# Optimization experiments

Measured on AMD Instinct MI355X. Metric: run time of the kernel, lower is better.

The kernel has to match this reference:

```python
import jax, jax.numpy as jnp
import numpy as np
from itertools import product

DIM = 384
HEADS = 8
DIM_HEAD = 64
INNER = HEADS * DIM_HEAD  # 512
KS = 3                    # kernel_size (attention window)
PAD = KS // 2
W_WIN = KS * KS           # 9
SCALE = DIM_HEAD ** -0.5


def setup_inputs() -> dict:
    key = jax.random.key(0)
    k1, k2, k3, k4, k5 = jax.random.split(key, 5)
    B, H, W = 4, 56, 56
    x = jax.random.normal(k1, (B, DIM, H, W), dtype=jnp.float32)
    # 1x1 conv weights stored as (out_ch, in_ch)
    Wq = jax.random.normal(k2, (INNER, DIM), dtype=jnp.float32) * (DIM ** -0.5)
    Wkv = jax.random.normal(k3, (2 * INNER, DIM), dtype=jnp.float32) * (DIM ** -0.5)
    Wo = jax.random.normal(k4, (DIM, INNER), dtype=jnp.float32) * (INNER ** -0.5)
    bo = jax.random.normal(k5, (DIM,), dtype=jnp.float32) * 0.01
    return {"x": x, "Wq": Wq, "Wkv": Wkv, "Wo": Wo, "bo": bo}


def _conv1x1(x, w):
    # x: (B,Cin,H,W), w: (Cout,Cin) -> (B,Cout,H,W)
    return jnp.einsum('bchw,oc->bohw', x, w)


def reference(x, Wq, Wkv, Wo, bo):
    B, C, H, W = x.shape
    q = _conv1x1(x, Wq)                       # (B, INNER, H, W)
    kv = _conv1x1(x, Wkv)                     # (B, 2*INNER, H, W)
    k, v = jnp.split(kv, 2, axis=1)
    # split channels heads-major, matching torch reshape (B, heads, dh, H, W)
    q = q.reshape(B, HEADS, DIM_HEAD, H, W)
    k = k.reshape(B, HEADS, DIM_HEAD, H, W)
    v = v.reshape(B, HEADS, DIM_HEAD, H, W)
    # zero-pad spatial dims (matches F.unfold zero padding: padded taps get logit 0)
    k_pad = jnp.pad(k, ((0, 0), (0, 0), (0, 0), (PAD, PAD), (PAD, PAD)))
    v_pad = jnp.pad(v, ((0, 0), (0, 0), (0, 0), (PAD, PAD), (PAD, PAD)))
    offsets = list(product(range(KS), range(KS)))  # row-major = unfold order
    # dots: (B, heads, H, W, w)
    dots = jnp.stack([
        jnp.einsum('bhdxy,bhdxy->bhxy', q, k_pad[:, :, :, i:i + H, j:j + W])
        for (i, j) in offsets
    ], axis=-1) * SCALE
    attn = jax.nn.softmax(dots, axis=-1)      # softmax over the 9-tap window
    # weighted sum of shifted v: (B, heads, dh, H, W)
    out = sum(
        attn[:, :, None, :, :, w_idx] * v_pad[:, :, :, i:i + H, j:j + W]
        for w_idx, (i, j) in enumerate(offsets)
    )
    out = out.reshape(B, INNER, H, W)
    return _conv1x1(out, Wo) + bo[None, :, None, None]
```

## Files before the change

### kernel.cpp

```cpp
#include <hip/hip_runtime.h>


#define HW 3136
#define WIMG 56
#define QKV_CH 1536
#define SCALE 0.125f
#define SLEN 200

typedef __bf16 bf16x8_t __attribute__((ext_vector_type(8)));
typedef float f32x4_t __attribute__((ext_vector_type(4)));

__device__ __forceinline__ float bf2f(unsigned short u) {
    return __uint_as_float(((unsigned int)u) << 16);
}
__device__ __forceinline__ unsigned short f2bf(float f) {
    unsigned int u = __float_as_uint(f);
    u += 0x7FFFu + ((u >> 16) & 1u);
    return (unsigned short)(u >> 16);
}

__global__ __launch_bounds__(256) void cvt_w(
    const float* __restrict__ Wq, const float* __restrict__ Wkv,
    const float* __restrict__ Wo,
    unsigned short* __restrict__ wT, unsigned short* __restrict__ wT3)
{
    const int i = blockIdx.x * 256 + threadIdx.x;
    if (i < 73728) {
        const int g = i & 3;
        const int idx3 = i >> 2;
        const int o128 = idx3 & 127;
        const int rest = idx3 >> 7;
        const int kb = rest % 12, oblk = rest / 12;
        const int o = oblk * 128 + o128;
        const int k0 = kb * 32 + g * 8;
        const float* src = (o < 512) ? (Wq + (size_t)o * 384 + k0)
                                     : (Wkv + (size_t)(o - 512) * 384 + k0);
        const float4 v0 = *reinterpret_cast<const float4*>(src);
        const float4 v1 = *reinterpret_cast<const float4*>(src + 4);
        uint4 u;
        u.x = (unsigned int)f2bf(v0.x) | ((unsigned int)f2bf(v0.y) << 16);
        u.y = (unsigned int)f2bf(v0.z) | ((unsigned int)f2bf(v0.w) << 16);
        u.z = (unsigned int)f2bf(v1.x) | ((unsigned int)f2bf(v1.y) << 16);
        u.w = (unsigned int)f2bf(v1.z) | ((unsigned int)f2bf(v1.w) << 16);
        reinterpret_cast<uint4*>(wT)[i] = u;
    } else {
        const int j = i - 73728;
        const int g = j & 3;
        const int idx3 = j >> 2;
        const int o128 = idx3 & 127;
        const int rest = idx3 >> 7;
        const int kb = rest % 16, oblk = rest / 16;
        const int o = oblk * 128 + o128;
        const float* src = Wo + (size_t)o * 512 + kb * 32 + g * 8;
        const float4 v0 = *reinterpret_cast<const float4*>(src);
        const float4 v1 = *reinterpret_cast<const float4*>(src + 4);
        uint4 u;
        u.x = (unsigned int)f2bf(v0.x) | ((unsigned int)f2bf(v0.y) << 16);
        u.y = (unsigned int)f2bf(v0.z) | ((unsigned int)f2bf(v0.w) << 16);
        u.z = (unsigned int)f2bf(v1.x) | ((unsigned int)f2bf(v1.y) << 16);
        u.w = (unsigned int)f2bf(v1.z) | ((unsigned int)f2bf(v1.w) << 16);
        reinterpret_cast<uint4*>(wT3)[j] = u;
    }
}

__global__ __launch_bounds__(256) void cvtT_x(
    const float* __restrict__ x, unsigned short* __restrict__ xT)
{
    __shared__ unsigned short Tl[64 * 36];
    const int sblk = blockIdx.x, kblk = blockIdx.y, b = blockIdx.z;
    const int t = threadIdx.x;

    if (sblk == 49) {
        unsigned short* dst = xT + (((size_t)b * 25 + 24) * 12 + kblk) * 4096 + 2048;
        *reinterpret_cast<uint4*>(dst + t * 8) = (uint4){0, 0, 0, 0};
        return;
    }

    const float* xp = x + ((size_t)b * 384 + (size_t)kblk * 32) * HW + sblk * 64;
    const int c = t >> 3;
#pragma unroll
    for (int i = 0; i < 2; i++) {
        const int sc = (t & 7) + 8 * i;
        const float4 v = *reinterpret_cast<const float4*>(xp + (size_t)c * HW + sc * 4);
        const int s4 = sc * 4;
        Tl[(s4 + 0) * 36 + c] = f2bf(v.x);
        Tl[(s4 + 1) * 36 + c] = f2bf(v.y);
        Tl[(s4 + 2) * 36 + c] = f2bf(v.z);
        Tl[(s4 + 3) * 36 + c] = f2bf(v.w);
    }
    __syncthreads();

    const int row = t >> 2, gran = t & 3;
    const uint2 lo = *reinterpret_cast<const uint2*>(&Tl[row * 36 + gran * 8]);
    const uint2 hi = *reinterpret_cast<const uint2*>(&Tl[row * 36 + gran * 8 + 4]);
    uint4 o; o.x = lo.x; o.y = lo.y; o.z = hi.x; o.w = hi.y;
    unsigned short* dst = xT + (((size_t)b * 25 + (sblk >> 1)) * 12 + kblk) * 4096
                        + (sblk & 1) * 2048;
    *reinterpret_cast<uint4*>(dst + t * 8) = o;
}

__global__ __launch_bounds__(256) void gemm1(
    const unsigned short* __restrict__ xT,
    const unsigned short* __restrict__ wT,
    unsigned short* __restrict__ qkv)
{
    __shared__ __align__(16) unsigned short A_lds[128 * 32];
    __shared__ __align__(16) unsigned short B_lds[128 * 32];

    const int sblk = blockIdx.x;
    const int oblk = blockIdx.y;
    const int b  = blockIdx.z;
    const int t  = threadIdx.x;
    const int lane = t & 63, w = t >> 6;
    const int quad = lane >> 4, mrow = lane & 15;
    const int wm = w >> 1, wn = w & 1;

    const unsigned short* wsrc = wT + ((size_t)oblk * 12) * 4096;
    const unsigned short* xsrc = xT + (((size_t)b * 25 + sblk) * 12) * 4096;

    f32x4_t acc[4][4];
#pragma unroll
    for (int m = 0; m < 4; m++)
#pragma unroll
        for (int n = 0; n < 4; n++) acc[m][n] = (f32x4_t){0.f, 0.f, 0.f, 0.f};

    for (int kb = 0; kb < 12; kb++) {
        const uint4 a0 = *reinterpret_cast<const uint4*>(wsrc + (size_t)kb * 4096 + t * 8);
        const uint4 a1 = *reinterpret_cast<const uint4*>(wsrc + (size_t)kb * 4096 + 2048 + t * 8);
        const uint4 b0 = *reinterpret_cast<const uint4*>(xsrc + (size_t)kb * 4096 + t * 8);
        const uint4 b1 = *reinterpret_cast<const uint4*>(xsrc + (size_t)kb * 4096 + 2048 + t * 8);

        __syncthreads();
        *reinterpret_cast<uint4*>(A_lds + t * 8) = a0;
        *reinterpret_cast<uint4*>(A_lds + 2048 + t * 8) = a1;
        *reinterpret_cast<uint4*>(B_lds + t * 8) = b0;
        *reinterpret_cast<uint4*>(B_lds + 2048 + t * 8) = b1;
        __syncthreads();

        bf16x8_t af[4], bf[4];
#pragma unroll
        for (int m = 0; m < 4; m++)
            af[m] = *reinterpret_cast<const bf16x8_t*>(&A_lds[(wm * 64 + m * 16 + mrow) * 32 + quad * 8]);
#pragma unroll
        for (int n = 0; n < 4; n++)
            bf[n] = *reinterpret_cast<const bf16x8_t*>(&B_lds[(wn * 64 + n * 16 + mrow) * 32 + quad * 8]);
#pragma unroll
        for (int m = 0; m < 4; m++)
#pragma unroll
            for (int n = 0; n < 4; n++)
                acc[m][n] = __builtin_amdgcn_mfma_f32_16x16x32_bf16(af[m], bf[n], acc[m][n], 0, 0, 0);
    }

    const int o0 = oblk * 128 + wm * 64;
    const int s0 = sblk * 128 + wn * 64;
    unsigned short* outb = qkv + (size_t)b * QKV_CH * HW;
#pragma unroll
    for (int m = 0; m < 4; m++)
#pragma unroll
        for (int n = 0; n < 4; n++) {
            const int ss = s0 + n * 16 + mrow;
            if (ss < HW) {
#pragma unroll
                for (int r = 0; r < 4; r++) {
                    const int oo = o0 + m * 16 + quad * 4 + r;
                    outb[(size_t)oo * HW + ss] = f2bf(acc[m][n][r]);
                }
            }
        }
}

__global__ __launch_bounds__(256) void natt2(
    const unsigned short* __restrict__ qkv,
    unsigned short* __restrict__ aoT)
{
    __shared__ __align__(16) unsigned short smem[2 * 64 * SLEN];
    unsigned short* Kl = smem;
    unsigned short* Vl = smem + 64 * SLEN;
    float* dred = reinterpret_cast<float*>(smem);

    const int t = threadIdx.x, lane = t & 63, w = t >> 6;
    const int sblk = blockIdx.x;
    const int s0 = sblk * 64;
    const int s  = s0 + lane;
    const int h  = blockIdx.y, b = blockIdx.z;
    const int y  = s / WIMG, xx = s % WIMG;

    const size_t hbase = (size_t)b * QKV_CH * HW + (size_t)(h * 64) * HW;
    const unsigned short* kg = qkv + hbase + (size_t)512 * HW;
    const unsigned short* vg = qkv + hbase + (size_t)1024 * HW;

#pragma unroll
    for (int i = 0; i < 6; i++) {
        const int f = i * 256 + t;
        const int d = f / 24, j = f % 24;
        int g = s0 - 64 + j * 8;
        g = min(max(g, 0), HW - 8);
        const uint4 k4 = *reinterpret_cast<const uint4*>(kg + (size_t)d * HW + g);
        const uint4 v4 = *reinterpret_cast<const uint4*>(vg + (size_t)d * HW + g);
        *reinterpret_cast<uint4*>(&Kl[d * SLEN + j * 8]) = k4;
        *reinterpret_cast<uint4*>(&Vl[d * SLEN + j * 8]) = v4;
    }

    int   off9[9];
    float msk[9];
#pragma unroll
    for (int ty = 0; ty < 3; ty++)
#pragma unroll
        for (int tx = 0; tx < 3; tx++) {
            const int tap = ty * 3 + tx;
            const int ny = y + ty - 1, nx = xx + tx - 1;
            const bool v = (ny >= 0) && (ny < WIMG) && (nx >= 0) && (nx < WIMG);
            off9[tap] = v ? ((ty - 1) * WIMG + (tx - 1)) : 0;
            msk[tap]  = v ? 1.f : 0.f;
        }

    __syncthreads();

    const unsigned short* qp = qkv + hbase + s;
    float dots[9];
#pragma unroll
    for (int tp = 0; tp < 9; tp++) dots[tp] = 0.f;
#pragma unroll 4
    for (int dd = 0; dd < 16; dd++) {
        const int d = w * 16 + dd;
        const float qv = bf2f(qp[(size_t)d * HW]);
        const int bi = d * SLEN + lane + 64;
#pragma unroll
        for (int tp = 0; tp < 9; tp++)
            dots[tp] += qv * bf2f(Kl[bi + off9[tp]]);
    }

    __syncthreads();
#pragma unroll
    for (int tp = 0; tp < 9; tp++) dred[(tp * 4 + w) * 64 + lane] = dots[tp];
    __syncthreads();

    float mx = -1e30f, dt[9];
#pragma unroll
    for (int tp = 0; tp < 9; tp++) {
        const float sum = dred[(tp * 4 + 0) * 64 + lane] + dred[(tp * 4 + 1) * 64 + lane] +
                          dred[(tp * 4 + 2) * 64 + lane] + dred[(tp * 4 + 3) * 64 + lane];
        dt[tp] = msk[tp] * (sum * SCALE);
        mx = fmaxf(mx, dt[tp]);
    }
    float se = 0.f, w9[9];
#pragma unroll
    for (int tp = 0; tp < 9; tp++) { w9[tp] = __expf(dt[tp] - mx); se += w9[tp]; }
    const float inv = 1.f / se;
#pragma unroll
    for (int tp = 0; tp < 9; tp++) w9[tp] *= inv * msk[tp];

    __align__(16) unsigned short ov[16];
#pragma unroll 4
    for (int dd = 0; dd < 16; dd++) {
        const int d = w * 16 + dd;
        const int bi = d * SLEN + lane + 64;
        float o = 0.f;
#pragma unroll
        for (int tp = 0; tp < 9; tp++)
            o += w9[tp] * bf2f(Vl[bi + off9[tp]]);
        ov[dd] = f2bf(o);
    }
    unsigned short* dst = aoT + (((size_t)(b * 49 + sblk)) * 16 + (h * 2 + (w >> 1))) * 2048
                        + lane * 32 + (w & 1) * 16;
    *reinterpret_cast<uint4*>(dst)     = *reinterpret_cast<const uint4*>(ov);
    *reinterpret_cast<uint4*>(dst + 8) = *reinterpret_cast<const uint4*>(ov + 8);
}

__global__ __launch_bounds__(256) void gemm3(
    const unsigned short* __restrict__ aoT,
    const unsigned short* __restrict__ wT3,
    const float* __restrict__ bias,
    float* __restrict__ out)
{
    __shared__ __align__(16) unsigned short A_lds[128 * 32];
    __shared__ __align__(16) unsigned short B_lds[64 * 32];

    const int sblk = blockIdx.x;
    const int oblk = blockIdx.y;
    const int b  = blockIdx.z;
    const int t  = threadIdx.x;
    const int lane = t & 63, w = t >> 6;
    const int quad = lane >> 4, mrow = lane & 15;
    const int wm = w >> 1, wn = w & 1;

    const unsigned short* asrc = wT3 + (size_t)oblk * 16 * 4096;
    const unsigned short* bsrc = aoT + ((size_t)(b * 49 + sblk)) * 16 * 2048;

    f32x4_t acc[4][2];
#pragma unroll
    for (int m = 0; m < 4; m++)
#pragma unroll
        for (int n = 0; n < 2; n++) acc[m][n] = (f32x4_t){0.f, 0.f, 0.f, 0.f};

    for (int kb = 0; kb < 16; kb++) {
        const uint4 a0 = *reinterpret_cast<const uint4*>(asrc + (size_t)kb * 4096 + t * 8);
        const uint4 a1 = *reinterpret_cast<const uint4*>(asrc + (size_t)kb * 4096 + 2048 + t * 8);
        const uint4 b0 = *reinterpret_cast<const uint4*>(bsrc + (size_t)kb * 2048 + t * 8);

        __syncthreads();
        *reinterpret_cast<uint4*>(A_lds + t * 8) = a0;
        *reinterpret_cast<uint4*>(A_lds + 2048 + t * 8) = a1;
        *reinterpret_cast<uint4*>(B_lds + t * 8) = b0;
        __syncthreads();

        bf16x8_t af[4], bf[2];
#pragma unroll
        for (int m = 0; m < 4; m++)
            af[m] = *reinterpret_cast<const bf16x8_t*>(&A_lds[(wm * 64 + m * 16 + mrow) * 32 + quad * 8]);
#pragma unroll
        for (int n = 0; n < 2; n++)
            bf[n] = *reinterpret_cast<const bf16x8_t*>(&B_lds[(wn * 32 + n * 16 + mrow) * 32 + quad * 8]);
#pragma unroll
        for (int m = 0; m < 4; m++)
#pragma unroll
            for (int n = 0; n < 2; n++)
                acc[m][n] = __builtin_amdgcn_mfma_f32_16x16x32_bf16(af[m], bf[n], acc[m][n], 0, 0, 0);
    }

    const int o0 = oblk * 128 + wm * 64;
    const int s0 = sblk * 64 + wn * 32;
    float* outb = out + (size_t)b * 384 * HW;
#pragma unroll
    for (int m = 0; m < 4; m++)
#pragma unroll
        for (int n = 0; n < 2; n++) {
            const int ss = s0 + n * 16 + mrow;
#pragma unroll
            for (int r = 0; r < 4; r++) {
                const int oo = o0 + m * 16 + quad * 4 + r;
                outb[(size_t)oo * HW + ss] = acc[m][n][r] + bias[oo];
            }
        }
}

extern "C" void kernel_launch(void* const* d_in, const int* in_sizes, int n_in,
                              void* d_out, int out_size, void* d_ws, size_t ws_size,
                              hipStream_t stream) {
    const float* x   = (const float*)d_in[0];
    const float* Wq  = (const float*)d_in[1];
    const float* Wkv = (const float*)d_in[2];
    const float* Wo  = (const float*)d_in[3];
    const float* bo  = (const float*)d_in[4];
    float* out = (float*)d_out;

    unsigned short* xT   = (unsigned short*)d_ws;
    unsigned short* wT   = xT + (size_t)4915200;
    unsigned short* wT3  = wT + (size_t)589824;
    unsigned short* qkvb = wT3 + (size_t)196608;
    unsigned short* aoT  = qkvb + (size_t)4 * QKV_CH * HW;

    cvt_w<<<dim3(384), 256, 0, stream>>>(Wq, Wkv, Wo, wT, wT3);
    cvtT_x<<<dim3(50, 12, 4), 256, 0, stream>>>(x, xT);

    gemm1<<<dim3(25, 12, 4), 256, 0, stream>>>(xT, wT, qkvb);
    natt2<<<dim3(49, 8, 4), 256, 0, stream>>>(qkvb, aoT);
    gemm3<<<dim3(49, 3, 4), 256, 0, stream>>>(aoT, wT3, bo, out);
}
```

Before: 145.5 us.

## Store K/V spatial-major, fuse conversion kernels, widen gemm3 tile

Result: slower. 148.5 us (+2.1%).

```diff
diff --git a/kernel.cpp b/kernel.cpp
--- a/kernel.cpp
+++ b/kernel.cpp
@@ -3,9 +3,8 @@
 
 #define HW 3136
 #define WIMG 56
-#define QKV_CH 1536
 #define SCALE 0.125f
-#define SLEN 200
+#define NROW 33
 
 typedef __bf16 bf16x8_t __attribute__((ext_vector_type(8)));
 typedef float f32x4_t __attribute__((ext_vector_type(4)));
@@ -13,18 +12,55 @@
 __device__ __forceinline__ float bf2f(unsigned short u) {
     return __uint_as_float(((unsigned int)u) << 16);
 }
+__device__ __forceinline__ float blo(unsigned int c) { return __uint_as_float(c << 16); }
+__device__ __forceinline__ float bhi(unsigned int c) { return __uint_as_float(c & 0xFFFF0000u); }
 __device__ __forceinline__ unsigned short f2bf(float f) {
     unsigned int u = __float_as_uint(f);
     u += 0x7FFFu + ((u >> 16) & 1u);
     return (unsigned short)(u >> 16);
 }
 
-__global__ __launch_bounds__(256) void cvt_w(
-    const float* __restrict__ Wq, const float* __restrict__ Wkv,
-    const float* __restrict__ Wo,
-    unsigned short* __restrict__ wT, unsigned short* __restrict__ wT3)
+__global__ __launch_bounds__(256) void cvt_all(
+    const float* __restrict__ x, const float* __restrict__ Wq,
+    const float* __restrict__ Wkv, const float* __restrict__ Wo,
+    unsigned short* __restrict__ xT, unsigned short* __restrict__ wT,
+    unsigned short* __restrict__ wT3)
 {
-    const int i = blockIdx.x * 256 + threadIdx.x;
+    __shared__ unsigned short Tl[64 * 36];
+    const int bid = blockIdx.x;
+    const int t = threadIdx.x;
+
+    if (bid < 2400) {
+        const int sblk = bid % 50, kblk = (bid / 50) % 12, b = bid / 600;
+        if (sblk == 49) {
+            unsigned short* dst = xT + (((size_t)b * 25 + 24) * 12 + kblk) * 4096 + 2048;
+            *reinterpret_cast<uint4*>(dst + t * 8) = (uint4){0, 0, 0, 0};
+            return;
+        }
+        const float* xp = x + ((size_t)b * 384 + (size_t)kblk * 32) * HW + sblk * 64;
+        const int c = t >> 3;
+#pragma unroll
+        for (int i = 0; i < 2; i++) {
+            const int sc = (t & 7) + 8 * i;
+            const float4 v = *reinterpret_cast<const float4*>(xp + (size_t)c * HW + sc * 4);
+            const int s4 = sc * 4;
+            Tl[(s4 + 0) * 36 + c] = f2bf(v.x);
+            Tl[(s4 + 1) * 36 + c] = f2bf(v.y);
+            Tl[(s4 + 2) * 36 + c] = f2bf(v.z);
+            Tl[(s4 + 3) * 36 + c] = f2bf(v.w);
+        }
+        __syncthreads();
+        const int row = t >> 2, gran = t & 3;
+        const uint2 lo = *reinterpret_cast<const uint2*>(&Tl[row * 36 + gran * 8]);
+        const uint2 hi = *reinterpret_cast<const uint2*>(&Tl[row * 36 + gran * 8 + 4]);
+        uint4 o; o.x = lo.x; o.y = lo.y; o.z = hi.x; o.w = hi.y;
+        unsigned short* dst = xT + (((size_t)b * 25 + (sblk >> 1)) * 12 + kblk) * 4096
+                            + (sblk & 1) * 2048;
+        *reinterpret_cast<uint4*>(dst + t * 8) = o;
+        return;
+    }
+
+    const int i = (bid - 2400) * 256 + t;
     if (i < 73728) {
         const int g = i & 3;
         const int idx3 = i >> 2;
@@ -63,46 +99,12 @@
     }
 }
 
-__global__ __launch_bounds__(256) void cvtT_x(
-    const float* __restrict__ x, unsigned short* __restrict__ xT)
-{
-    __shared__ unsigned short Tl[64 * 36];
-    const int sblk = blockIdx.x, kblk = blockIdx.y, b = blockIdx.z;
-    const int t = threadIdx.x;
-
-    if (sblk == 49) {
-        unsigned short* dst = xT + (((size_t)b * 25 + 24) * 12 + kblk) * 4096 + 2048;
-        *reinterpret_cast<uint4*>(dst + t * 8) = (uint4){0, 0, 0, 0};
-        return;
-    }
-
-    const float* xp = x + ((size_t)b * 384 + (size_t)kblk * 32) * HW + sblk * 64;
-    const int c = t >> 3;
-#pragma unroll
-    for (int i = 0; i < 2; i++) {
-        const int sc = (t & 7) + 8 * i;
-        const float4 v = *reinterpret_cast<const float4*>(xp + (size_t)c * HW + sc * 4);
-        const int s4 = sc * 4;
-        Tl[(s4 + 0) * 36 + c] = f2bf(v.x);
-        Tl[(s4 + 1) * 36 + c] = f2bf(v.y);
-        Tl[(s4 + 2) * 36 + c] = f2bf(v.z);
-        Tl[(s4 + 3) * 36 + c] = f2bf(v.w);
-    }
-    __syncthreads();
-
-    const int row = t >> 2, gran = t & 3;
-    const uint2 lo = *reinterpret_cast<const uint2*>(&Tl[row * 36 + gran * 8]);
-    const uint2 hi = *reinterpret_cast<const uint2*>(&Tl[row * 36 + gran * 8 + 4]);
-    uint4 o; o.x = lo.x; o.y = lo.y; o.z = hi.x; o.w = hi.y;
-    unsigned short* dst = xT + (((size_t)b * 25 + (sblk >> 1)) * 12 + kblk) * 4096
-                        + (sblk & 1) * 2048;
-    *reinterpret_cast<uint4*>(dst + t * 8) = o;
-}
-
 __global__ __launch_bounds__(256) void gemm1(
     const unsigned short* __restrict__ xT,
     const unsigned short* __restrict__ wT,
-    unsigned short* __restrict__ qkv)
+    unsigned short* __restrict__ qb,
+    unsigned short* __restrict__ kT,
+    unsigned short* __restrict__ vT)
 {
     __shared__ __align__(16) unsigned short A_lds[128 * 32];
     __shared__ __align__(16) unsigned short B_lds[128 * 32];
@@ -153,30 +155,51 @@
 
     const int o0 = oblk * 128 + wm * 64;
     const int s0 = sblk * 128 + wn * 64;
-    unsigned short* outb = qkv + (size_t)b * QKV_CH * HW;
-#pragma unroll
-    for (int m = 0; m < 4; m++)
-#pragma unroll
-        for (int n = 0; n < 4; n++) {
-            const int ss = s0 + n * 16 + mrow;
-            if (ss < HW) {
-#pragma unroll
-                for (int r = 0; r < 4; r++) {
-                    const int oo = o0 + m * 16 + quad * 4 + r;
-                    outb[(size_t)oo * HW + ss] = f2bf(acc[m][n][r]);
+    if (o0 < 512) {
+        unsigned short* outb = qb + (size_t)b * 512 * HW;
+#pragma unroll
+        for (int m = 0; m < 4; m++)
+#pragma unroll
+            for (int n = 0; n < 4; n++) {
+                const int ss = s0 + n * 16 + mrow;
+                if (ss < HW) {
+#pragma unroll
+                    for (int r = 0; r < 4; r++)
+                        outb[(size_t)(o0 + m * 16 + quad * 4 + r) * HW + ss] = f2bf(acc[m][n][r]);
                 }
             }
-        }
-}
-
-__global__ __launch_bounds__(256) void natt2(
-    const unsigned short* __restrict__ qkv,
+    } else {
+        const int rel = o0 - 512;
+        unsigned short* base = (rel < 512) ? kT : vT;
+        const int h = (rel & 511) >> 6;
+        unsigned short* hb = base + (size_t)(b * 8 + h) * HW * 64;
+#pragma unroll
+        for (int m = 0; m < 4; m++) {
+            const int d0 = m * 16 + quad * 4;
+#pragma unroll
+            for (int n = 0; n < 4; n++) {
+                const int ss = s0 + n * 16 + mrow;
+                if (ss < HW) {
+                    uint2 u;
+                    u.x = (unsigned int)f2bf(acc[m][n][0]) | ((unsigned int)f2bf(acc[m][n][1]) << 16);
+                    u.y = (unsigned int)f2bf(acc[m][n][2]) | ((unsigned int)f2bf(acc[m][n][3]) << 16);
+                    *reinterpret_cast<uint2*>(hb + (size_t)ss * 64 + d0) = u;
+                }
+            }
+        }
+    }
+}
+
+__global__ __launch_bounds__(256) void natt4(
+    const unsigned short* __restrict__ qb,
+    const unsigned short* __restrict__ kT,
+    const unsigned short* __restrict__ vT,
     unsigned short* __restrict__ aoT)
 {
-    __shared__ __align__(16) unsigned short smem[2 * 64 * SLEN];
-    unsigned short* Kl = smem;
-    unsigned short* Vl = smem + 64 * SLEN;
-    float* dred = reinterpret_cast<float*>(smem);
+    __shared__ __align__(16) unsigned int KV[2 * 192 * NROW];
+    unsigned int* Kl = KV;
+    unsigned int* Vl = KV + 192 * NROW;
+    float* dred = reinterpret_cast<float*>(KV);
 
     const int t = threadIdx.x, lane = t & 63, w = t >> 6;
     const int sblk = blockIdx.x;
@@ -185,23 +208,22 @@
     const int h  = blockIdx.y, b = blockIdx.z;
     const int y  = s / WIMG, xx = s % WIMG;
 
-    const size_t hbase = (size_t)b * QKV_CH * HW + (size_t)(h * 64) * HW;
-    const unsigned short* kg = qkv + hbase + (size_t)512 * HW;
-    const unsigned short* vg = qkv + hbase + (size_t)1024 * HW;
+    const unsigned short* kg = kT + (size_t)(b * 8 + h) * HW * 64;
+    const unsigned short* vg = vT + (size_t)(b * 8 + h) * HW * 64;
 
 #pragma unroll
     for (int i = 0; i < 6; i++) {
         const int f = i * 256 + t;
-        const int d = f / 24, j = f % 24;
-        int g = s0 - 64 + j * 8;
-        g = min(max(g, 0), HW - 8);
-        const uint4 k4 = *reinterpret_cast<const uint4*>(kg + (size_t)d * HW + g);
-        const uint4 v4 = *reinterpret_cast<const uint4*>(vg + (size_t)d * HW + g);
-        *reinterpret_cast<uint4*>(&Kl[d * SLEN + j * 8]) = k4;
-        *reinterpret_cast<uint4*>(&Vl[d * SLEN + j * 8]) = v4;
-    }
-
-    int   off9[9];
+        const int row = f >> 3, col4 = f & 7;
+        const int sg = min(max(s0 - 64 + row, 0), HW - 1);
+        const uint4 k4 = *reinterpret_cast<const uint4*>(kg + (size_t)sg * 64 + col4 * 8);
+        const uint4 v4 = *reinterpret_cast<const uint4*>(vg + (size_t)sg * 64 + col4 * 8);
+        const int db = row * NROW + col4 * 4;
+        Kl[db] = k4.x; Kl[db + 1] = k4.y; Kl[db + 2] = k4.z; Kl[db + 3] = k4.w;
+        Vl[db] = v4.x; Vl[db + 1] = v4.y; Vl[db + 2] = v4.z; Vl[db + 3] = v4.w;
+    }
+
+    int   off33[9];
     float msk[9];
 #pragma unroll
     for (int ty = 0; ty < 3; ty++)
@@ -210,24 +232,29 @@
             const int tap = ty * 3 + tx;
             const int ny = y + ty - 1, nx = xx + tx - 1;
             const bool v = (ny >= 0) && (ny < WIMG) && (nx >= 0) && (nx < WIMG);
-            off9[tap] = v ? ((ty - 1) * WIMG + (tx - 1)) : 0;
+            off33[tap] = (v ? ((ty - 1) * WIMG + (tx - 1)) : 0) * NROW;
             msk[tap]  = v ? 1.f : 0.f;
         }
 
     __syncthreads();
 
-    const unsigned short* qp = qkv + hbase + s;
+    const unsigned short* qp = qb + (size_t)b * 512 * HW + (size_t)(h * 64) * HW + s;
+    const int rb0 = (lane + 64) * NROW;
     float dots[9];
 #pragma unroll
     for (int tp = 0; tp < 9; tp++) dots[tp] = 0.f;
 #pragma unroll 4
-    for (int dd = 0; dd < 16; dd++) {
-        const int d = w * 16 + dd;
-        const float qv = bf2f(qp[(size_t)d * HW]);
-        const int bi = d * SLEN + lane + 64;
-#pragma unroll
-        for (int tp = 0; tp < 9; tp++)
-            dots[tp] += qv * bf2f(Kl[bi + off9[tp]]);
+    for (int j = 0; j < 8; j++) {
+        const int p = w * 8 + j;
+        const float q0 = bf2f(qp[(size_t)(2 * p) * HW]);
+        const float q1 = bf2f(qp[(size_t)(2 * p + 1) * HW]);
+        const int rb = rb0 + p;
+#pragma unroll
+        for (int tp = 0; tp < 9; tp++) {
+            const unsigned int c = Kl[rb + off33[tp]];
+            dots[tp] += q0 * blo(c);
+            dots[tp] += q1 * bhi(c);
+        }
     }
 
     __syncthreads();
@@ -252,14 +279,17 @@
 
     __align__(16) unsigned short ov[16];
 #pragma unroll 4
-    for (int dd = 0; dd < 16; dd++) {
-        const int d = w * 16 + dd;
-        const int bi = d * SLEN + lane + 64;
-        float o = 0.f;
-#pragma unroll
-        for (int tp = 0; tp < 9; tp++)
-            o += w9[tp] * bf2f(Vl[bi + off9[tp]]);
-        ov[dd] = f2bf(o);
+    for (int j = 0; j < 8; j++) {
+        const int rb = rb0 + w * 8 + j;
+        float olo = 0.f, ohi = 0.f;
+#pragma unroll
+        for (int tp = 0; tp < 9; tp++) {
+            const unsigned int c = Vl[rb + off33[tp]];
+            olo += w9[tp] * blo(c);
+            ohi += w9[tp] * bhi(c);
+        }
+        ov[2 * j]     = f2bf(olo);
+        ov[2 * j + 1] = f2bf(ohi);
     }
     unsigned short* dst = aoT + (((size_t)(b * 49 + sblk)) * 16 + (h * 2 + (w >> 1))) * 2048
                         + lane * 32 + (w & 1) * 16;
@@ -274,7 +304,7 @@
     float* __restrict__ out)
 {
     __shared__ __align__(16) unsigned short A_lds[128 * 32];
-    __shared__ __align__(16) unsigned short B_lds[64 * 32];
+    __shared__ __align__(16) unsigned short B_lds[128 * 32];
 
     const int sblk = blockIdx.x;
     const int oblk = blockIdx.y;
@@ -284,52 +314,58 @@
     const int quad = lane >> 4, mrow = lane & 15;
     const int wm = w >> 1, wn = w & 1;
 
+    const int t0 = 2 * sblk, t1 = min(2 * sblk + 1, 48);
     const unsigned short* asrc = wT3 + (size_t)oblk * 16 * 4096;
-    const unsigned short* bsrc = aoT + ((size_t)(b * 49 + sblk)) * 16 * 2048;
-
-    f32x4_t acc[4][2];
+    const unsigned short* bsrc0 = aoT + ((size_t)(b * 49 + t0)) * 16 * 2048;
+    const unsigned short* bsrc1 = aoT + ((size_t)(b * 49 + t1)) * 16 * 2048;
+
+    f32x4_t acc[4][4];
 #pragma unroll
     for (int m = 0; m < 4; m++)
 #pragma unroll
-        for (int n = 0; n < 2; n++) acc[m][n] = (f32x4_t){0.f, 0.f, 0.f, 0.f};
+        for (int n = 0; n < 4; n++) acc[m][n] = (f32x4_t){0.f, 0.f, 0.f, 0.f};
 
     for (int kb = 0; kb < 16; kb++) {
         const uint4 a0 = *reinterpret_cast<const uint4*>(asrc + (size_t)kb * 4096 + t * 8);
         const uint4 a1 = *reinterpret_cast<const uint4*>(asrc + (size_t)kb * 4096 + 2048 + t * 8);
-        const uint4 b0 = *reinterpret_cast<const uint4*>(bsrc + (size_t)kb * 2048 + t * 8);
+        const uint4 b0 = *reinterpret_cast<const uint4*>(bsrc0 + (size_t)kb * 2048 + t * 8);
+        const uint4 b1 = *reinterpret_cast<const uint4*>(bsrc1 + (size_t)kb * 2048 + t * 8);
 
         __syncthreads();
         *reinterpret_cast<uint4*>(A_lds + t * 8) = a0;
         *reinterpret_cast<uint4*>(A_lds + 2048 + t * 8) = a1;
         *reinterpret_cast<uint4*>(B_lds + t * 8) = b0;
-        __syncthreads();
-
-        bf16x8_t af[4], bf[2];
+        *reinterpret_cast<uint4*>(B_lds + 2048 + t * 8) = b1;
+        __syncthreads();
+
+        bf16x8_t af[4], bf[4];
 #pragma unroll
         for (int m = 0; m < 4; m++)
             af[m] = *reinterpret_cast<const bf16x8_t*>(&A_lds[(wm * 64 + m * 16 + mrow) * 32 + quad * 8]);
 #pragma unroll
-        for (int n = 0; n < 2; n++)
-            bf[n] = *reinterpret_cast<const bf16x8_t*>(&B_lds[(wn * 32 + n * 16 + mrow) * 32 + quad * 8]);
-#pragma unroll
-        for (int m = 0; m < 4; m++)
-#pragma unroll
-            for (int n = 0; n < 2; n++)
+        for (int n = 0; n < 4; n++)
+            bf[n] = *reinterpret_cast<const bf16x8_t*>(&B_lds[(wn * 64 + n * 16 + mrow) * 32 + quad * 8]);
+#pragma unroll
+        for (int m = 0; m < 4; m++)
+#pragma unroll
+            for (int n = 0; n < 4; n++)
                 acc[m][n] = __builtin_amdgcn_mfma_f32_16x16x32_bf16(af[m], bf[n], acc[m][n], 0, 0, 0);
     }
 
     const int o0 = oblk * 128 + wm * 64;
-    const int s0 = sblk * 64 + wn * 32;
+    const int s0 = sblk * 128 + wn * 64;
     float* outb = out + (size_t)b * 384 * HW;
 #pragma unroll
     for (int m = 0; m < 4; m++)
 #pragma unroll
-        for (int n = 0; n < 2; n++) {
+        for (int n = 0; n < 4; n++) {
             const int ss = s0 + n * 16 + mrow;
-#pragma unroll
-            for (int r = 0; r < 4; r++) {
-                const int oo = o0 + m * 16 + quad * 4 + r;
-                outb[(size_t)oo * HW + ss] = acc[m][n][r] + bias[oo];
+            if (ss < HW) {
+#pragma unroll
+                for (int r = 0; r < 4; r++) {
+                    const int oo = o0 + m * 16 + quad * 4 + r;
+                    outb[(size_t)oo * HW + ss] = acc[m][n][r] + bias[oo];
+                }
             }
         }
 }
@@ -344,16 +380,16 @@
     const float* bo  = (const float*)d_in[4];
     float* out = (float*)d_out;
 
-    unsigned short* xT   = (unsigned short*)d_ws;
-    unsigned short* wT   = xT + (size_t)4915200;
-    unsigned short* wT3  = wT + (size_t)589824;
-    unsigned short* qkvb = wT3 + (size_t)196608;
-    unsigned short* aoT  = qkvb + (size_t)4 * QKV_CH * HW;
-
-    cvt_w<<<dim3(384), 256, 0, stream>>>(Wq, Wkv, Wo, wT, wT3);
-    cvtT_x<<<dim3(50, 12, 4), 256, 0, stream>>>(x, xT);
-
-    gemm1<<<dim3(25, 12, 4), 256, 0, stream>>>(xT, wT, qkvb);
-    natt2<<<dim3(49, 8, 4), 256, 0, stream>>>(qkvb, aoT);
-    gemm3<<<dim3(49, 3, 4), 256, 0, stream>>>(aoT, wT3, bo, out);
-}
+    unsigned short* xT  = (unsigned short*)d_ws;
+    unsigned short* wT  = xT + (size_t)4915200;
+    unsigned short* wT3 = wT + (size_t)589824;
+    unsigned short* qb  = wT3 + (size_t)196608;
+    unsigned short* kT  = qb + (size_t)6422528;
+    unsigned short* vT  = kT + (size_t)6422528;
+    unsigned short* aoT = vT + (size_t)6422528;
+
+    cvt_all<<<dim3(2784), 256, 0, stream>>>(x, Wq, Wkv, Wo, xT, wT, wT3);
+    gemm1<<<dim3(25, 12, 4), 256, 0, stream>>>(xT, wT, qb, kT, vT);
+    natt4<<<dim3(49, 8, 4), 256, 0, stream>>>(qb, kT, vT, aoT);
+    gemm3<<<dim3(25, 3, 4), 256, 0, stream>>>(aoT, wT3, bo, out);
+}
```
